# Kernel tuning notes

Measured on AMD Instinct MI355X. Metric: run time of the kernel, lower is better.

Reference implementation:

```python
import jax, jax.numpy as jnp
import numpy as np

N_HEAD = 16
ROPE_BASE = 10000.0


def _rope_cos_sin(T, D, dtype):
    # D = head_size; matches RotaryEmbedding: emb = cat(freqs, freqs)
    inv_freq = 1.0 / (ROPE_BASE ** (jnp.arange(0, D, 2, dtype=jnp.float32) / D))
    t = jnp.arange(T, dtype=jnp.float32)
    freqs = t[:, None] * inv_freq[None, :]              # [T, D/2]
    emb = jnp.concatenate([freqs, freqs], axis=-1)      # [T, D]
    return jnp.cos(emb).astype(dtype), jnp.sin(emb).astype(dtype)


def _rotate_half(x):
    d = x.shape[-1] // 2
    return jnp.concatenate([-x[..., d:], x[..., :d]], axis=-1)


def setup_inputs() -> dict:
    key = jax.random.key(0)
    ks = jax.random.split(key, 5)
    B, T, C = 2, 2048, 1024
    s_in = 1.0 / np.sqrt(C)
    return {
        "x": jax.random.normal(ks[0], (B, T, C), dtype=jnp.float32),
        "w_attn": jax.random.normal(ks[1], (C, 3 * C), dtype=jnp.float32) * s_in,
        "b_attn": jnp.zeros((3 * C,), dtype=jnp.float32),
        "w_proj": jax.random.normal(ks[2], (C, C), dtype=jnp.float32) * s_in,
        "b_proj": jnp.zeros((C,), dtype=jnp.float32),
    }


def reference(x, w_attn, b_attn, w_proj, b_proj):
    B, T, C = x.shape
    H = N_HEAD
    D = C // H

    qkv = x @ w_attn + b_attn                            # [B,T,3C]
    q, k, v = jnp.split(qkv, 3, axis=-1)
    # [B,T,C] -> [B,H,T,D]
    to_heads = lambda a: a.reshape(B, T, H, D).transpose(0, 2, 1, 3)
    q, k, v = to_heads(q), to_heads(k), to_heads(v)

    cos, sin = _rope_cos_sin(T, D, x.dtype)              # [T,D] each, broadcast over B,H
    q = q * cos + _rotate_half(q) * sin
    k = k * cos + _rotate_half(k) * sin

    scale = 1.0 / np.sqrt(D)
    att = jnp.einsum("bhqd,bhkd->bhqk", q, k) * scale    # [B,H,T,T]
    causal = jnp.tril(jnp.ones((T, T), dtype=bool))
    att = jnp.where(causal, att, jnp.finfo(att.dtype).min)
    att = jax.nn.softmax(att, axis=-1)
    y = jnp.einsum("bhqk,bhkd->bhqd", att, v)            # [B,H,T,D]

    y = y.transpose(0, 2, 1, 3).reshape(B, T, C)
    return y @ w_proj + b_proj
```

## Files before the change

kernel.cpp:

```cpp
#include <hip/hip_runtime.h>
#include <hip/hip_bf16.h>

#define B_ 2
#define T_ 2048
#define C_ 1024
#define H_ 16
#define D_ 64

typedef __attribute__((ext_vector_type(8))) short bf16x8;
typedef __attribute__((ext_vector_type(4))) float f32x4;

static __device__ __forceinline__ float bf2f(unsigned short u) {
  union { unsigned int i; float f; } c;
  c.i = ((unsigned int)u) << 16;
  return c.f;
}
static __device__ __forceinline__ unsigned short f2bf(float f) {
  union { float f; unsigned int i; } c;
  c.f = f;
  unsigned int x = c.i;
  return (unsigned short)((x + 0x7fffu + ((x >> 16) & 1u)) >> 16);
}

static __device__ __forceinline__ void gl_lds16(const void* g, void* s) {
  __builtin_amdgcn_global_load_lds(
      (const __attribute__((address_space(1))) void*)g,
      (__attribute__((address_space(3))) void*)s, 16, 0, 0);
}

__global__ __launch_bounds__(256) void fill_kernel_f32(float* __restrict__ out,
                                                       int n, float v) {
  int i = blockIdx.x * 256 + threadIdx.x;
  if (i < n) out[i] = v;
}

__global__ __launch_bounds__(256) void cvt_bf16(const float* __restrict__ X,
                                                unsigned short* __restrict__ Xb) {
  int i = (blockIdx.x * 256 + threadIdx.x) * 8;
  float4 f0 = *(const float4*)(X + i);
  float4 f1 = *(const float4*)(X + i + 4);
  union { unsigned short u[8]; uint4 v; } p;
  p.u[0] = f2bf(f0.x); p.u[1] = f2bf(f0.y); p.u[2] = f2bf(f0.z); p.u[3] = f2bf(f0.w);
  p.u[4] = f2bf(f1.x); p.u[5] = f2bf(f1.y); p.u[6] = f2bf(f1.z); p.u[7] = f2bf(f1.w);
  *(uint4*)(Xb + i) = p.v;
}

__global__ __launch_bounds__(256) void transpose_cvt(const float* __restrict__ W,
                                                     unsigned short* __restrict__ WT,
                                                     int Kd, int Nd) {
  __shared__ float tile[32][33];
  const int n0 = blockIdx.x * 32, k0 = blockIdx.y * 32;
  const int tx = threadIdx.x & 31, ty = threadIdx.x >> 5;
#pragma unroll
  for (int i = 0; i < 4; ++i)
    tile[ty + i * 8][tx] = W[(size_t)(k0 + ty + i * 8) * Nd + n0 + tx];
  __syncthreads();
#pragma unroll
  for (int i = 0; i < 4; ++i)
    WT[(size_t)(n0 + ty + i * 8) * Kd + k0 + tx] = f2bf(tile[tx][ty + i * 8]);
}

__global__ __launch_bounds__(256) void v_transpose(const unsigned short* __restrict__ vP,
                                                   unsigned short* __restrict__ vT) {
  __shared__ unsigned short tile[64][72];
  const int t0 = blockIdx.x * 64;
  const int bh = blockIdx.y;
  const int b = bh >> 4;
  const int srow = threadIdx.x >> 3;
  const int sc8 = (threadIdx.x & 7) * 8;
#pragma unroll
  for (int it = 0; it < 2; ++it) {
    int r = srow + it * 32;
    *(uint4*)&tile[r][sc8] =
        *(const uint4*)(vP + (size_t)(b * T_ + t0 + r) * 1024 + (bh & 15) * 64 + sc8);
  }
  __syncthreads();
#pragma unroll
  for (int it = 0; it < 2; ++it) {
    int dd = srow + it * 32;
    union { unsigned short u[8]; uint4 v; } o;
#pragma unroll
    for (int j = 0; j < 8; ++j) o.u[j] = tile[sc8 + j][dd];
    *(uint4*)(vT + ((size_t)bh * 64 + dd) * 2048 + t0 + sc8) = o.v;
  }
}

template <int OUT_PLANES>
__global__ __launch_bounds__(256) void mfma_gemm(
    const unsigned short* __restrict__ A,
    const unsigned short* __restrict__ BT,
    const float* __restrict__ bias,
    unsigned short* __restrict__ qP, unsigned short* __restrict__ kP,
    unsigned short* __restrict__ vP, float* __restrict__ Fout,
    int N, int K) {
  __shared__ unsigned short As[128 * 64];
  __shared__ unsigned short Bs[128 * 64];

  const int tid = threadIdx.x;
  const int w = tid >> 6, lane = tid & 63;
  const int lo = lane & 15, g = lane >> 4;
  const int wm = (w >> 1) * 64, wn = (w & 1) * 64;
  const int m0 = blockIdx.y * 128, n0 = blockIdx.x * 128;

  const int lr8 = lane >> 3;

  const f32x4 zero4 = {0.f, 0.f, 0.f, 0.f};
  f32x4 acc[4][4] = {{zero4, zero4, zero4, zero4}, {zero4, zero4, zero4, zero4},
                     {zero4, zero4, zero4, zero4}, {zero4, zero4, zero4, zero4}};

  for (int k0 = 0; k0 < K; k0 += 64) {
    __syncthreads();
#pragma unroll
    for (int it = 0; it < 4; ++it) {
      const int base_row = w * 32 + it * 8;
      const int r = base_row + lr8;
      const int j = (lane & 7) ^ (r & 7);
      gl_lds16(A + (size_t)(m0 + r) * K + k0 + j * 8, &As[base_row * 64]);
      gl_lds16(BT + (size_t)(n0 + r) * K + k0 + j * 8, &Bs[base_row * 64]);
    }
    __syncthreads();

#pragma unroll
    for (int kk = 0; kk < 2; ++kk) {
      bf16x8 af[4], bfr[4];
#pragma unroll
      for (int i = 0; i < 4; ++i) {
        int ra = wm + i * 16 + lo;
        int rb = wn + i * 16 + lo;
        af[i]  = *(const bf16x8*)&As[ra * 64 + ((g + kk * 4) ^ (ra & 7)) * 8];
        bfr[i] = *(const bf16x8*)&Bs[rb * 64 + ((g + kk * 4) ^ (rb & 7)) * 8];
      }
#pragma unroll
      for (int i = 0; i < 4; ++i)
#pragma unroll
        for (int j = 0; j < 4; ++j)
          acc[i][j] = __builtin_amdgcn_mfma_f32_16x16x32_bf16(af[i], bfr[j],
                                                              acc[i][j], 0, 0, 0);
    }
  }

  float bv[4];
#pragma unroll
  for (int j = 0; j < 4; ++j) bv[j] = bias[n0 + wn + j * 16 + lo];

  if (OUT_PLANES) {
    const int pl = n0 >> 10;
    unsigned short* P = (pl == 0) ? qP : (pl == 1) ? kP : vP;
    const int col0 = (n0 & 1023) + wn + lo;
#pragma unroll
    for (int i = 0; i < 4; ++i)
#pragma unroll
      for (int r = 0; r < 4; ++r) {
        size_t row = (size_t)(m0 + wm + i * 16 + g * 4 + r);
#pragma unroll
        for (int j = 0; j < 4; ++j)
          P[row * 1024 + col0 + j * 16] = f2bf(acc[i][j][r] + bv[j]);
      }
  } else {
#pragma unroll
    for (int i = 0; i < 4; ++i)
#pragma unroll
      for (int r = 0; r < 4; ++r) {
        size_t row = (size_t)(m0 + wm + i * 16 + g * 4 + r);
#pragma unroll
        for (int j = 0; j < 4; ++j)
          Fout[row * N + n0 + wn + j * 16 + lo] = acc[i][j][r] + bv[j];
      }
  }
}

__global__ __launch_bounds__(256) void rope_kernel(unsigned short* __restrict__ qP,
                                                   unsigned short* __restrict__ kP) {
  int idx = blockIdx.x * 256 + threadIdx.x;
  int i = idx & 31;
  int h = (idx >> 5) & 15;
  int t = (idx >> 9) & 2047;
  int b = idx >> 20;
  float inv = exp2f((float)(-2 * i) * (13.287712379549449f / 64.0f));
  float ang = (float)t * inv;
  float s, c;
  sincosf(ang, &s, &c);
  size_t base = (size_t)(b * T_ + t) * 1024 + h * D_ + i;
  float q1 = bf2f(qP[base]);
  float q2 = bf2f(qP[base + 32]);
  qP[base]      = f2bf((q1 * c - q2 * s) * 0.125f);
  qP[base + 32] = f2bf((q2 * c + q1 * s) * 0.125f);
  float k1 = bf2f(kP[base]);
  float k2 = bf2f(kP[base + 32]);
  kP[base]      = f2bf(k1 * c - k2 * s);
  kP[base + 32] = f2bf(k2 * c + k1 * s);
}

__global__ __launch_bounds__(256) void flash_mfma6(
    unsigned short* __restrict__ qP,
    const unsigned short* __restrict__ kP,
    const unsigned short* __restrict__ vT) {
  const int bx = blockIdx.x;
  const int bh = blockIdx.y;
  const int b = bh >> 4, h = bh & 15;
  const int tid = threadIdx.x;
  const int w = tid >> 6, lane = tid & 63;
  const int lo = lane & 15, g = lane >> 4;

  __shared__ unsigned short Ks[64][72];
  __shared__ unsigned short VTs[64][72];
  __shared__ unsigned short Ps[64][72];

  const int srow = tid >> 3;
  const int sc8 = (tid & 7) * 8;
  const f32x4 zero4 = {0.f, 0.f, 0.f, 0.f};

#pragma unroll
  for (int half = 0; half < 2; ++half) {
    const int qt = half ? (31 - bx) : bx;
    const int rowq0 = b * T_ + qt * 64;

    const unsigned short* qrow = qP + (size_t)(rowq0 + w * 16 + lo) * 1024 + h * 64;
    bf16x8 aq0 = *(const bf16x8*)(qrow + g * 8);
    bf16x8 aq1 = *(const bf16x8*)(qrow + 32 + g * 8);

    f32x4 oacc[4] = {zero4, zero4, zero4, zero4};
    float lsum = 0.f;

    uint4 kreg0, kreg1, vreg0, vreg1;
    {
      const size_t kb = (size_t)(b * T_ + srow) * 1024 + h * 64 + sc8;
      kreg0 = *(const uint4*)(kP + kb);
      kreg1 = *(const uint4*)(kP + kb + (size_t)32 * 1024);
      const size_t vb = ((size_t)bh * 64 + srow) * 2048 + sc8;
      vreg0 = *(const uint4*)(vT + vb);
      vreg1 = *(const uint4*)(vT + vb + (size_t)32 * 2048);
    }

    for (int kt = 0; kt <= qt; ++kt) {
      __syncthreads();
      *(uint4*)&Ks[srow][sc8]       = kreg0;
      *(uint4*)&Ks[srow + 32][sc8]  = kreg1;
      *(uint4*)&VTs[srow][sc8]      = vreg0;
      *(uint4*)&VTs[srow + 32][sc8] = vreg1;
      __syncthreads();
      if (kt < qt) {
        const size_t kb = (size_t)(b * T_ + (kt + 1) * 64 + srow) * 1024 + h * 64 + sc8;
        kreg0 = *(const uint4*)(kP + kb);
        kreg1 = *(const uint4*)(kP + kb + (size_t)32 * 1024);
        const size_t vb = ((size_t)bh * 64 + srow) * 2048 + (kt + 1) * 64 + sc8;
        vreg0 = *(const uint4*)(vT + vb);
        vreg1 = *(const uint4*)(vT + vb + (size_t)32 * 2048);
      }

      f32x4 sacc[4] = {zero4, zero4, zero4, zero4};
      __builtin_amdgcn_s_setprio(1);
#pragma unroll
      for (int ct = 0; ct < 4; ++ct) {
        bf16x8 bk0 = *(const bf16x8*)&Ks[ct * 16 + lo][g * 8];
        bf16x8 bk1 = *(const bf16x8*)&Ks[ct * 16 + lo][32 + g * 8];
        sacc[ct] = __builtin_amdgcn_mfma_f32_16x16x32_bf16(bk0, aq0, sacc[ct], 0, 0, 0);
        sacc[ct] = __builtin_amdgcn_mfma_f32_16x16x32_bf16(bk1, aq1, sacc[ct], 0, 0, 0);
      }
      __builtin_amdgcn_s_setprio(0);

      if (kt == qt) {
#pragma unroll
        for (int ct = 0; ct < 4; ++ct)
#pragma unroll
          for (int r = 0; r < 4; ++r)
            if (ct * 16 + g * 4 + r > w * 16 + lo) sacc[ct][r] = -1e30f;
      }

#pragma unroll
      for (int ct = 0; ct < 4; ++ct) {
        float p0 = __expf(sacc[ct][0]);
        float p1 = __expf(sacc[ct][1]);
        float p2 = __expf(sacc[ct][2]);
        float p3 = __expf(sacc[ct][3]);
        lsum += (p0 + p1) + (p2 + p3);
        unsigned int u0 = (unsigned int)f2bf(p0) | ((unsigned int)f2bf(p1) << 16);
        unsigned int u1 = (unsigned int)f2bf(p2) | ((unsigned int)f2bf(p3) << 16);
        uint2 pw; pw.x = u0; pw.y = u1;
        *(uint2*)&Ps[w * 16 + lo][ct * 16 + g * 4] = pw;
      }

      bf16x8 ap0 = *(const bf16x8*)&Ps[w * 16 + lo][g * 8];
      bf16x8 ap1 = *(const bf16x8*)&Ps[w * 16 + lo][32 + g * 8];
      __builtin_amdgcn_s_setprio(1);
#pragma unroll
      for (int c2 = 0; c2 < 4; ++c2) {
        bf16x8 bv0 = *(const bf16x8*)&VTs[c2 * 16 + lo][g * 8];
        bf16x8 bv1 = *(const bf16x8*)&VTs[c2 * 16 + lo][32 + g * 8];
        oacc[c2] = __builtin_amdgcn_mfma_f32_16x16x32_bf16(ap0, bv0, oacc[c2], 0, 0, 0);
        oacc[c2] = __builtin_amdgcn_mfma_f32_16x16x32_bf16(ap1, bv1, oacc[c2], 0, 0, 0);
      }
      __builtin_amdgcn_s_setprio(0);
    }

    lsum += __shfl_xor(lsum, 16);
    lsum += __shfl_xor(lsum, 32);

#pragma unroll
    for (int r = 0; r < 4; ++r) {
      float inv_r = 1.0f / __shfl(lsum, g * 4 + r);
      unsigned short* dst = qP + (size_t)(rowq0 + w * 16 + g * 4 + r) * 1024 + h * 64 + lo;
#pragma unroll
      for (int c2 = 0; c2 < 4; ++c2)
        dst[c2 * 16] = f2bf(oacc[c2][r] * inv_r);
    }
  }
}

extern "C" void kernel_launch(void* const* d_in, const int* in_sizes, int n_in,
                              void* d_out, int out_size, void* d_ws, size_t ws_size,
                              hipStream_t stream) {
  const float *x = nullptr, *w_attn = nullptr, *b_attn = nullptr,
              *w_proj = nullptr, *b_proj = nullptr;
  for (int i = 0; i < n_in; ++i) {
    switch (in_sizes[i]) {
      case B_ * T_ * C_:  x      = (const float*)d_in[i]; break;
      case C_ * 3 * C_:   w_attn = (const float*)d_in[i]; break;
      case 3 * C_:        b_attn = (const float*)d_in[i]; break;
      case C_ * C_:       w_proj = (const float*)d_in[i]; break;
      case C_:            b_proj = (const float*)d_in[i]; break;
      default: break;
    }
  }
  float* out = (float*)d_out;
  const int nblk = (out_size + 255) / 256;

  if (!x || !w_attn || !b_attn || !w_proj || !b_proj) {
    fill_kernel_f32<<<nblk, 256, 0, stream>>>(out, out_size, 100.0f);
    return;
  }
  if (ws_size < (size_t)48 * 1024 * 1024) {
    fill_kernel_f32<<<nblk, 256, 0, stream>>>(out, out_size, 50.0f);
    return;
  }

  unsigned short* qP  = (unsigned short*)d_ws;
  unsigned short* kP  = qP + (size_t)(B_ * T_) * 1024;
  unsigned short* vP  = kP + (size_t)(B_ * T_) * 1024;
  unsigned short* vT  = vP + (size_t)(B_ * T_) * 1024;
  unsigned short* xb  = vT + (size_t)(B_ * T_) * 1024;
  unsigned short* waT = xb + (size_t)(B_ * T_) * C_;
  unsigned short* wpT = waT + (size_t)C_ * 3 * C_;

  transpose_cvt<<<dim3((3 * C_) / 32, C_ / 32), 256, 0, stream>>>(w_attn, waT, C_, 3 * C_);
  transpose_cvt<<<dim3(C_ / 32, C_ / 32), 256, 0, stream>>>(w_proj, wpT, C_, C_);
  cvt_bf16<<<(B_ * T_ * C_) / (256 * 8), 256, 0, stream>>>(x, xb);
  mfma_gemm<1><<<dim3((3 * C_) / 128, (B_ * T_) / 128), 256, 0, stream>>>(
      xb, waT, b_attn, qP, kP, vP, nullptr, 3 * C_, C_);
  rope_kernel<<<(B_ * T_ * H_ * (D_ / 2)) / 256, 256, 0, stream>>>(qP, kP);
  v_transpose<<<dim3(T_ / 64, B_ * H_), 256, 0, stream>>>(vP, vT);
  flash_mfma6<<<dim3(16, B_ * H_), 256, 0, stream>>>(qP, kP, vT);
  mfma_gemm<0><<<dim3(C_ / 128, (B_ * T_) / 128), 256, 0, stream>>>(
      qP, wpT, b_proj, nullptr, nullptr, nullptr, out, C_, C_);
}
```

Baseline: 196.7 us.

## Load K/V fragments directly from global memory and remap blocks per XCD

The flash attention kernel no longer stages K and V tiles through shared memory with register prefetch and two barriers per iteration. Each wave now reads its MFMA operands straight from global memory and relies on L2/MALL caching. The grid is flattened and remapped so that all blocks of the same four heads land on one XCD, which improves L2 locality for shared K/V. The risk is that four waves redundantly fetch the same K/V data and global-load latency is now exposed without explicit prefetch.

```diff
diff --git a/kernel.cpp b/kernel.cpp
--- a/kernel.cpp
+++ b/kernel.cpp
@@ -191,24 +191,26 @@
   kP[base + 32] = f2bf(k2 * c + k1 * s);
 }
 
-__global__ __launch_bounds__(256) void flash_mfma6(
+__global__ __launch_bounds__(256) void flash_mfma7(
     unsigned short* __restrict__ qP,
     const unsigned short* __restrict__ kP,
     const unsigned short* __restrict__ vT) {
-  const int bx = blockIdx.x;
-  const int bh = blockIdx.y;
+  const int cid = blockIdx.x;
+  const int xcd = cid & 7;
+  const int k6 = cid >> 3;
+  const int bh = xcd * 4 + (k6 >> 4);
+  const int bx = k6 & 15;
   const int b = bh >> 4, h = bh & 15;
   const int tid = threadIdx.x;
   const int w = tid >> 6, lane = tid & 63;
   const int lo = lane & 15, g = lane >> 4;
 
-  __shared__ unsigned short Ks[64][72];
-  __shared__ unsigned short VTs[64][72];
   __shared__ unsigned short Ps[64][72];
 
-  const int srow = tid >> 3;
-  const int sc8 = (tid & 7) * 8;
   const f32x4 zero4 = {0.f, 0.f, 0.f, 0.f};
+
+  const unsigned short* kbase = kP + (size_t)b * T_ * 1024 + h * 64;
+  const unsigned short* vbase = vT + (size_t)bh * 64 * 2048;
 
 #pragma unroll
   for (int half = 0; half < 2; ++half) {
@@ -222,38 +224,14 @@
     f32x4 oacc[4] = {zero4, zero4, zero4, zero4};
     float lsum = 0.f;
 
-    uint4 kreg0, kreg1, vreg0, vreg1;
-    {
-      const size_t kb = (size_t)(b * T_ + srow) * 1024 + h * 64 + sc8;
-      kreg0 = *(const uint4*)(kP + kb);
-      kreg1 = *(const uint4*)(kP + kb + (size_t)32 * 1024);
-      const size_t vb = ((size_t)bh * 64 + srow) * 2048 + sc8;
-      vreg0 = *(const uint4*)(vT + vb);
-      vreg1 = *(const uint4*)(vT + vb + (size_t)32 * 2048);
-    }
-
     for (int kt = 0; kt <= qt; ++kt) {
-      __syncthreads();
-      *(uint4*)&Ks[srow][sc8]       = kreg0;
-      *(uint4*)&Ks[srow + 32][sc8]  = kreg1;
-      *(uint4*)&VTs[srow][sc8]      = vreg0;
-      *(uint4*)&VTs[srow + 32][sc8] = vreg1;
-      __syncthreads();
-      if (kt < qt) {
-        const size_t kb = (size_t)(b * T_ + (kt + 1) * 64 + srow) * 1024 + h * 64 + sc8;
-        kreg0 = *(const uint4*)(kP + kb);
-        kreg1 = *(const uint4*)(kP + kb + (size_t)32 * 1024);
-        const size_t vb = ((size_t)bh * 64 + srow) * 2048 + (kt + 1) * 64 + sc8;
-        vreg0 = *(const uint4*)(vT + vb);
-        vreg1 = *(const uint4*)(vT + vb + (size_t)32 * 2048);
-      }
-
       f32x4 sacc[4] = {zero4, zero4, zero4, zero4};
       __builtin_amdgcn_s_setprio(1);
 #pragma unroll
       for (int ct = 0; ct < 4; ++ct) {
-        bf16x8 bk0 = *(const bf16x8*)&Ks[ct * 16 + lo][g * 8];
-        bf16x8 bk1 = *(const bf16x8*)&Ks[ct * 16 + lo][32 + g * 8];
+        const unsigned short* kr = kbase + (size_t)(kt * 64 + ct * 16 + lo) * 1024;
+        bf16x8 bk0 = *(const bf16x8*)(kr + g * 8);
+        bf16x8 bk1 = *(const bf16x8*)(kr + 32 + g * 8);
         sacc[ct] = __builtin_amdgcn_mfma_f32_16x16x32_bf16(bk0, aq0, sacc[ct], 0, 0, 0);
         sacc[ct] = __builtin_amdgcn_mfma_f32_16x16x32_bf16(bk1, aq1, sacc[ct], 0, 0, 0);
       }
@@ -285,8 +263,9 @@
       __builtin_amdgcn_s_setprio(1);
 #pragma unroll
       for (int c2 = 0; c2 < 4; ++c2) {
-        bf16x8 bv0 = *(const bf16x8*)&VTs[c2 * 16 + lo][g * 8];
-        bf16x8 bv1 = *(const bf16x8*)&VTs[c2 * 16 + lo][32 + g * 8];
+        const unsigned short* vr = vbase + (size_t)(c2 * 16 + lo) * 2048 + kt * 64;
+        bf16x8 bv0 = *(const bf16x8*)(vr + g * 8);
+        bf16x8 bv1 = *(const bf16x8*)(vr + 32 + g * 8);
         oacc[c2] = __builtin_amdgcn_mfma_f32_16x16x32_bf16(ap0, bv0, oacc[c2], 0, 0, 0);
         oacc[c2] = __builtin_amdgcn_mfma_f32_16x16x32_bf16(ap1, bv1, oacc[c2], 0, 0, 0);
       }
@@ -349,7 +328,7 @@
       xb, waT, b_attn, qP, kP, vP, nullptr, 3 * C_, C_);
   rope_kernel<<<(B_ * T_ * H_ * (D_ / 2)) / 256, 256, 0, stream>>>(qP, kP);
   v_transpose<<<dim3(T_ / 64, B_ * H_), 256, 0, stream>>>(vP, vT);
-  flash_mfma6<<<dim3(16, B_ * H_), 256, 0, stream>>>(qP, kP, vT);
+  flash_mfma7<<<dim3(512), 256, 0, stream>>>(qP, kP, vT);
   mfma_gemm<0><<<dim3(C_ / 128, (B_ * T_) / 128), 256, 0, stream>>>(
       qP, wpT, b_proj, nullptr, nullptr, nullptr, out, C_, C_);
 }
```

Measured after the change: 273.2 us. +38.9%, slower.

## Enlarge flash attention query tile to 128 rows per block

Applied to the files above, without the earlier changes.

Each wave now handles two 16-row query sub-tiles, so a block covers 128 queries and reuses every staged K/V tile for twice as many rows. This halves the K/V global loads and LDS staging per query. The grid shrinks to 8x32 blocks (256 blocks) and register use roughly doubles, which lowers occupancy and parallelism. Causal masking now works per sub-tile, and the diagonal region spans two key tiles.

```diff
diff --git a/kernel.cpp b/kernel.cpp
--- a/kernel.cpp
+++ b/kernel.cpp
@@ -191,7 +191,7 @@
   kP[base + 32] = f2bf(k2 * c + k1 * s);
 }
 
-__global__ __launch_bounds__(256) void flash_mfma6(
+__global__ __launch_bounds__(256) void flash_mfma8(
     unsigned short* __restrict__ qP,
     const unsigned short* __restrict__ kP,
     const unsigned short* __restrict__ vT) {
@@ -204,7 +204,7 @@
 
   __shared__ unsigned short Ks[64][72];
   __shared__ unsigned short VTs[64][72];
-  __shared__ unsigned short Ps[64][72];
+  __shared__ unsigned short Ps[128][72];
 
   const int srow = tid >> 3;
   const int sc8 = (tid & 7) * 8;
@@ -212,15 +212,22 @@
 
 #pragma unroll
   for (int half = 0; half < 2; ++half) {
-    const int qt = half ? (31 - bx) : bx;
-    const int rowq0 = b * T_ + qt * 64;
-
-    const unsigned short* qrow = qP + (size_t)(rowq0 + w * 16 + lo) * 1024 + h * 64;
-    bf16x8 aq0 = *(const bf16x8*)(qrow + g * 8);
-    bf16x8 aq1 = *(const bf16x8*)(qrow + 32 + g * 8);
-
-    f32x4 oacc[4] = {zero4, zero4, zero4, zero4};
-    float lsum = 0.f;
+    const int qt = half ? (15 - bx) : bx;
+    const int rowq0 = b * T_ + qt * 128;
+    const int ktmax = 2 * qt + 1;
+
+    bf16x8 aq[2][2];
+#pragma unroll
+    for (int qs = 0; qs < 2; ++qs) {
+      const unsigned short* qrow =
+          qP + (size_t)(rowq0 + w * 32 + qs * 16 + lo) * 1024 + h * 64;
+      aq[qs][0] = *(const bf16x8*)(qrow + g * 8);
+      aq[qs][1] = *(const bf16x8*)(qrow + 32 + g * 8);
+    }
+
+    f32x4 oacc[2][4] = {{zero4, zero4, zero4, zero4},
+                        {zero4, zero4, zero4, zero4}};
+    float lsum[2] = {0.f, 0.f};
 
     uint4 kreg0, kreg1, vreg0, vreg1;
     {
@@ -232,14 +239,14 @@
       vreg1 = *(const uint4*)(vT + vb + (size_t)32 * 2048);
     }
 
-    for (int kt = 0; kt <= qt; ++kt) {
+    for (int kt = 0; kt <= ktmax; ++kt) {
       __syncthreads();
       *(uint4*)&Ks[srow][sc8]       = kreg0;
       *(uint4*)&Ks[srow + 32][sc8]  = kreg1;
       *(uint4*)&VTs[srow][sc8]      = vreg0;
       *(uint4*)&VTs[srow + 32][sc8] = vreg1;
       __syncthreads();
-      if (kt < qt) {
+      if (kt < ktmax) {
         const size_t kb = (size_t)(b * T_ + (kt + 1) * 64 + srow) * 1024 + h * 64 + sc8;
         kreg0 = *(const uint4*)(kP + kb);
         kreg1 = *(const uint4*)(kP + kb + (size_t)32 * 1024);
@@ -248,61 +255,86 @@
         vreg1 = *(const uint4*)(vT + vb + (size_t)32 * 2048);
       }
 
-      f32x4 sacc[4] = {zero4, zero4, zero4, zero4};
+      f32x4 sacc[2][4] = {{zero4, zero4, zero4, zero4},
+                          {zero4, zero4, zero4, zero4}};
       __builtin_amdgcn_s_setprio(1);
 #pragma unroll
       for (int ct = 0; ct < 4; ++ct) {
         bf16x8 bk0 = *(const bf16x8*)&Ks[ct * 16 + lo][g * 8];
         bf16x8 bk1 = *(const bf16x8*)&Ks[ct * 16 + lo][32 + g * 8];
-        sacc[ct] = __builtin_amdgcn_mfma_f32_16x16x32_bf16(bk0, aq0, sacc[ct], 0, 0, 0);
-        sacc[ct] = __builtin_amdgcn_mfma_f32_16x16x32_bf16(bk1, aq1, sacc[ct], 0, 0, 0);
+#pragma unroll
+        for (int qs = 0; qs < 2; ++qs) {
+          sacc[qs][ct] = __builtin_amdgcn_mfma_f32_16x16x32_bf16(bk0, aq[qs][0],
+                                                                 sacc[qs][ct], 0, 0, 0);
+          sacc[qs][ct] = __builtin_amdgcn_mfma_f32_16x16x32_bf16(bk1, aq[qs][1],
+                                                                 sacc[qs][ct], 0, 0, 0);
+        }
       }
       __builtin_amdgcn_s_setprio(0);
 
-      if (kt == qt) {
-#pragma unroll
-        for (int ct = 0; ct < 4; ++ct)
-#pragma unroll
-          for (int r = 0; r < 4; ++r)
-            if (ct * 16 + g * 4 + r > w * 16 + lo) sacc[ct][r] = -1e30f;
-      }
-
-#pragma unroll
-      for (int ct = 0; ct < 4; ++ct) {
-        float p0 = __expf(sacc[ct][0]);
-        float p1 = __expf(sacc[ct][1]);
-        float p2 = __expf(sacc[ct][2]);
-        float p3 = __expf(sacc[ct][3]);
-        lsum += (p0 + p1) + (p2 + p3);
-        unsigned int u0 = (unsigned int)f2bf(p0) | ((unsigned int)f2bf(p1) << 16);
-        unsigned int u1 = (unsigned int)f2bf(p2) | ((unsigned int)f2bf(p3) << 16);
-        uint2 pw; pw.x = u0; pw.y = u1;
-        *(uint2*)&Ps[w * 16 + lo][ct * 16 + g * 4] = pw;
-      }
-
-      bf16x8 ap0 = *(const bf16x8*)&Ps[w * 16 + lo][g * 8];
-      bf16x8 ap1 = *(const bf16x8*)&Ps[w * 16 + lo][32 + g * 8];
+#pragma unroll
+      for (int qs = 0; qs < 2; ++qs) {
+        if (kt * 64 + 63 > qt * 128 + w * 32 + qs * 16) {
+          const int qloc = qt * 128 + w * 32 + qs * 16 + lo;
+#pragma unroll
+          for (int ct = 0; ct < 4; ++ct)
+#pragma unroll
+            for (int r = 0; r < 4; ++r)
+              if (kt * 64 + ct * 16 + g * 4 + r > qloc) sacc[qs][ct][r] = -1e30f;
+        }
+      }
+
+#pragma unroll
+      for (int qs = 0; qs < 2; ++qs)
+#pragma unroll
+        for (int ct = 0; ct < 4; ++ct) {
+          float p0 = __expf(sacc[qs][ct][0]);
+          float p1 = __expf(sacc[qs][ct][1]);
+          float p2 = __expf(sacc[qs][ct][2]);
+          float p3 = __expf(sacc[qs][ct][3]);
+          lsum[qs] += (p0 + p1) + (p2 + p3);
+          unsigned int u0 = (unsigned int)f2bf(p0) | ((unsigned int)f2bf(p1) << 16);
+          unsigned int u1 = (unsigned int)f2bf(p2) | ((unsigned int)f2bf(p3) << 16);
+          uint2 pw; pw.x = u0; pw.y = u1;
+          *(uint2*)&Ps[w * 32 + qs * 16 + lo][ct * 16 + g * 4] = pw;
+        }
+
+      bf16x8 ap[2][2];
+#pragma unroll
+      for (int qs = 0; qs < 2; ++qs) {
+        ap[qs][0] = *(const bf16x8*)&Ps[w * 32 + qs * 16 + lo][g * 8];
+        ap[qs][1] = *(const bf16x8*)&Ps[w * 32 + qs * 16 + lo][32 + g * 8];
+      }
       __builtin_amdgcn_s_setprio(1);
 #pragma unroll
       for (int c2 = 0; c2 < 4; ++c2) {
         bf16x8 bv0 = *(const bf16x8*)&VTs[c2 * 16 + lo][g * 8];
         bf16x8 bv1 = *(const bf16x8*)&VTs[c2 * 16 + lo][32 + g * 8];
-        oacc[c2] = __builtin_amdgcn_mfma_f32_16x16x32_bf16(ap0, bv0, oacc[c2], 0, 0, 0);
-        oacc[c2] = __builtin_amdgcn_mfma_f32_16x16x32_bf16(ap1, bv1, oacc[c2], 0, 0, 0);
+#pragma unroll
+        for (int qs = 0; qs < 2; ++qs) {
+          oacc[qs][c2] = __builtin_amdgcn_mfma_f32_16x16x32_bf16(ap[qs][0], bv0,
+                                                                 oacc[qs][c2], 0, 0, 0);
+          oacc[qs][c2] = __builtin_amdgcn_mfma_f32_16x16x32_bf16(ap[qs][1], bv1,
+                                                                 oacc[qs][c2], 0, 0, 0);
+        }
       }
       __builtin_amdgcn_s_setprio(0);
     }
 
-    lsum += __shfl_xor(lsum, 16);
-    lsum += __shfl_xor(lsum, 32);
-
-#pragma unroll
-    for (int r = 0; r < 4; ++r) {
-      float inv_r = 1.0f / __shfl(lsum, g * 4 + r);
-      unsigned short* dst = qP + (size_t)(rowq0 + w * 16 + g * 4 + r) * 1024 + h * 64 + lo;
-#pragma unroll
-      for (int c2 = 0; c2 < 4; ++c2)
-        dst[c2 * 16] = f2bf(oacc[c2][r] * inv_r);
+#pragma unroll
+    for (int qs = 0; qs < 2; ++qs) {
+      float ls = lsum[qs];
+      ls += __shfl_xor(ls, 16);
+      ls += __shfl_xor(ls, 32);
+#pragma unroll
+      for (int r = 0; r < 4; ++r) {
+        float inv_r = 1.0f / __shfl(ls, g * 4 + r);
+        unsigned short* dst =
+            qP + (size_t)(rowq0 + w * 32 + qs * 16 + g * 4 + r) * 1024 + h * 64 + lo;
+#pragma unroll
+        for (int c2 = 0; c2 < 4; ++c2)
+          dst[c2 * 16] = f2bf(oacc[qs][c2][r] * inv_r);
+      }
     }
   }
 }
@@ -349,7 +381,7 @@
       xb, waT, b_attn, qP, kP, vP, nullptr, 3 * C_, C_);
   rope_kernel<<<(B_ * T_ * H_ * (D_ / 2)) / 256, 256, 0, stream>>>(qP, kP);
   v_transpose<<<dim3(T_ / 64, B_ * H_), 256, 0, stream>>>(vP, vT);
-  flash_mfma6<<<dim3(16, B_ * H_), 256, 0, stream>>>(qP, kP, vT);
+  flash_mfma8<<<dim3(8, B_ * H_), 256, 0, stream>>>(qP, kP, vT);
   mfma_gemm<0><<<dim3(C_ / 128, (B_ * T_) / 128), 256, 0, stream>>>(
       qP, wpT, b_proj, nullptr, nullptr, nullptr, out, C_, C_);
 }
```

After: 209.8 us. 6.7% more time.
